# Kernel optimization log

Measured on AMD Instinct MI355X. Metric: run time of the kernel, lower is better.

The kernel has to match this reference:

```python
import jax, jax.numpy as jnp
import numpy as np

U, T, K, Q, H = 4096, 200, 64, 10000, 128
STD_THETA = 1.0


def setup_inputs() -> dict:
    key = jax.random.key(0)
    ks = jax.random.split(key, 12)
    q_id = jax.random.randint(ks[0], (U, T), 0, Q, dtype=jnp.int32)
    resp = jax.random.randint(ks[1], (U, T), 0, 2, dtype=jnp.int32)
    # one KC per question so the per-timestep masked_select size is constant (= U)
    kc_of_q = jax.random.randint(ks[2], (Q,), 0, K)
    kmap = jax.nn.one_hot(kc_of_q, K, dtype=jnp.float32) > 0.5  # (Q, K) bool, one-hot
    mask = jnp.ones((U, T), dtype=bool)
    diff_mu = jax.random.normal(ks[3], (Q,), dtype=jnp.float32)
    disc_mu = jax.random.normal(ks[4], (Q,), dtype=jnp.float32)
    xav = lambda k, fi, fo: jax.random.normal(k, (fi, fo), dtype=jnp.float32) * (2.0 / (fi + fo)) ** 0.5
    W1 = xav(ks[5], 3, H)
    W2 = xav(ks[6], H, H)
    W3 = xav(ks[7], H, 2)
    b1 = jnp.zeros((H,), jnp.float32)
    b2 = jnp.zeros((H,), jnp.float32)
    b3 = jnp.zeros((2,), jnp.float32)
    return dict(mask=mask, q_id=q_id, kmap=kmap, resp=resp,
                diff_mu=diff_mu, disc_mu=disc_mu,
                W1=W1, b1=b1, W2=W2, b2=b2, W3=W3, b3=b3)


def reference(mask, q_id, kmap, resp, diff_mu, disc_mu, W1, b1, W2, b2, W3, b3):
    gelu = lambda x: jax.nn.gelu(x, approximate=False)  # torch nn.GELU default = exact erf
    nu = q_id.shape[0]
    td = diff_mu[q_id]                      # (U, T) trial difficulty
    ts = disc_mu[q_id]                      # (U, T) trial discrimination
    x = jnp.stack([td, ts, resp.astype(jnp.float32)], axis=-1)  # (U, T, 3)
    h = gelu(gelu(x @ W1 + b1) @ W2 + b2)
    out = gelu(h @ W3 + b3)                 # (U, T, 2)
    mu = out[..., 0].T                      # (T, U)
    logvar = out[..., 1].T                  # (T, U)
    std = jnp.maximum(jnp.exp(0.5 * logvar), 1e-8)
    r = (STD_THETA / std) ** 2              # (T, U)

    # backward Kalman-style recursion: b_t = 1/(1 + r_t + (1 - b_{t+1})), c_t = b_t*(c_{t+1} + r_t*mu_t)
    def bwd_step(carry, rm):
        b_n, c_n = carry
        r_t, mu_t = rm
        b_t = 1.0 / (1.0 + r_t + (1.0 - b_n))
        c_t = b_t * (c_n + r_t * mu_t)
        return (b_t, c_t), (b_t, c_t)

    init = (jnp.ones((nu,), mu.dtype), jnp.zeros((nu,), mu.dtype))
    _, (b_seq, c_seq) = jax.lax.scan(bwd_step, init, (r, mu), reverse=True)  # (T, U) each

    # forward pass: gather active-KC ability, update, scatter back into per-user KC state
    active_kc = jnp.argmax(kmap[q_id], axis=-1).T  # (T, U) one active KC per trial
    uidx = jnp.arange(nu)

    def fwd_step(curr, bck):
        b_t, c_t, kc_t = bck
        prev = curr[uidx, kc_t]
        mu_t = b_t * prev + c_t
        curr = curr.at[uidx, kc_t].set(mu_t)
        return curr, mu_t

    curr0 = jnp.zeros((nu, kmap.shape[1]), mu.dtype)
    last_ability_kc, ability_T = jax.lax.scan(fwd_step, curr0, (b_seq, c_seq, active_kc))
    ability = ability_T.T                   # (U, T): masked mean over one-hot KC = active KC ability
    trial_logits = ts * (ability - td)      # (U, T)
    return trial_logits, last_ability_kc
```

## Files before the change

### kernel.cpp

```cpp
#include <hip/hip_runtime.h>
#include <math.h>

#define U_ 4096
#define T_ 200
#define K_ 64
#define Q_ 10000
#define H_ 128

__device__ __forceinline__ float gelu_f(float x) {
  return 0.5f * x * (1.0f + erff(x * 0.70710678118654752440f));
}

__device__ __forceinline__ float rlanef(float v, int l) {
  return __int_as_float(__builtin_amdgcn_readlane(__float_as_int(v), l));
}
__device__ __forceinline__ int rlanei(int v, int l) {
  return __builtin_amdgcn_readlane(v, l);
}

__global__ __launch_bounds__(256, 4) void mlp_table_kernel(
    const float* __restrict__ diff_mu, const float* __restrict__ disc_mu,
    const float* __restrict__ W1, const float* __restrict__ b1,
    const float* __restrict__ W2, const float* __restrict__ b2,
    const float* __restrict__ W3, const float* __restrict__ b3,
    const unsigned char* __restrict__ kmap,
    float4* __restrict__ tab4, int* __restrict__ kc_of_q) {
  __shared__ float W2s[64 * H_];
  __shared__ float h1buf[16][H_];

  const int tid = threadIdx.x;
  const int base = blockIdx.x * 16;

  for (int v = tid; v < 64 * H_; v += 256) W2s[v] = W2[v];

  if (blockIdx.x < 40) {
    int q = blockIdx.x * 256 + tid;
    if (q < Q_) {
      const unsigned char* km = kmap + (size_t)q * K_;
      int kc = 0;
#pragma unroll
      for (int k = 0; k < K_; ++k)
        if (km[k]) kc = k;
      kc_of_q[q] = kc;
    }
  }

  for (int v = tid; v < 16 * H_; v += 256) {
    int pl = v >> 7, j = v & 127;
    int pg = base + pl;
    int q = pg >> 1;
    float rf = (float)(pg & 1);
    float td = diff_mu[q], ts = disc_mu[q];
    float a = b1[j];
    a += td * W1[j];
    a += ts * W1[H_ + j];
    a += rf * W1[2 * H_ + j];
    h1buf[pl][j] = gelu_f(a);
  }
  __syncthreads();

  const int w = tid >> 6, lane = tid & 63;
  float a0[4] = {0.f, 0.f, 0.f, 0.f}, a1[4] = {0.f, 0.f, 0.f, 0.f};
  const float* h1w = &h1buf[w * 4][0];

#pragma clang loop unroll_count(8)
  for (int k = 0; k < 64; ++k) {
    float w0 = W2s[k * H_ + lane];
    float w1 = W2s[k * H_ + lane + 64];
#pragma unroll
    for (int p = 0; p < 4; ++p) {
      float hv = h1w[p * H_ + k];
      a0[p] = fmaf(w0, hv, a0[p]);
      a1[p] = fmaf(w1, hv, a1[p]);
    }
  }
  __syncthreads();
  for (int v = tid; v < 64 * H_; v += 256) W2s[v] = W2[64 * H_ + v];
  __syncthreads();
#pragma clang loop unroll_count(8)
  for (int k = 0; k < 64; ++k) {
    float w0 = W2s[k * H_ + lane];
    float w1 = W2s[k * H_ + lane + 64];
#pragma unroll
    for (int p = 0; p < 4; ++p) {
      float hv = h1w[p * H_ + 64 + k];
      a0[p] = fmaf(w0, hv, a0[p]);
      a1[p] = fmaf(w1, hv, a1[p]);
    }
  }

  float w30a = W3[lane * 2 + 0], w31a = W3[lane * 2 + 1];
  float w30b = W3[(lane + 64) * 2 + 0], w31b = W3[(lane + 64) * 2 + 1];
  float b2a = b2[lane], b2b = b2[lane + 64];
  float b30 = b3[0], b31 = b3[1];
#pragma unroll
  for (int p = 0; p < 4; ++p) {
    float h2a = gelu_f(a0[p] + b2a);
    float h2b = gelu_f(a1[p] + b2b);
    float s0 = h2a * w30a + h2b * w30b;
    float s1 = h2a * w31a + h2b * w31b;
#pragma unroll
    for (int off = 32; off > 0; off >>= 1) {
      s0 += __shfl_xor(s0, off, 64);
      s1 += __shfl_xor(s1, off, 64);
    }
    if (lane == 0) {
      float mu = gelu_f(s0 + b30);
      float lv = gelu_f(s1 + b31);
      float sd = fmaxf(expf(0.5f * lv), 1e-8f);
      int pg = base + w * 4 + p;
      int q = pg >> 1;
      tab4[pg] = make_float4(1.0f / (sd * sd), mu, disc_mu[q], diff_mu[q]);
    }
  }
}

__global__ __launch_bounds__(256) void scan_kernel(
    const int* __restrict__ q_id, const int* __restrict__ resp,
    const float4* __restrict__ tab4, const int* __restrict__ kc_of_q,
    float* __restrict__ out) {
  const int lane = threadIdx.x & 63;
  const int u = (blockIdx.x << 2) | (threadIdx.x >> 6);

  float tr[4], tmu[4], tts[4], ttd[4];
  int tkc[4];
#pragma unroll
  for (int i = 0; i < 4; ++i) {
    int t = i * 64 + lane;
    int tc = t < T_ ? t : T_ - 1;
    int q = q_id[u * T_ + tc];
    int rp = resp[u * T_ + tc];
    float4 f = tab4[q * 2 + rp];
    tr[i] = f.x;
    tmu[i] = f.y;
    tts[i] = f.z;
    ttd[i] = f.w;
    tkc[i] = kc_of_q[q];
  }

  float b = 1.0f, c = 0.0f;
#define BWD_STEP(i, s)                                   \
  {                                                      \
    float r_ = rlanef(tr[i], s);                         \
    float m_ = rlanef(tmu[i], s);                        \
    float x_ = 2.0f + r_ - b;                            \
    float ib = __builtin_amdgcn_rcpf(x_);                \
    ib = ib * (2.0f - x_ * ib);         \
    b = ib;                                              \
    c = b * fmaf(r_, m_, c);                             \
    tr[i] = (lane == (s)) ? b : tr[i];                   \
    tmu[i] = (lane == (s)) ? c : tmu[i];                 \
  }
#pragma unroll
  for (int s = 7; s >= 0; --s) BWD_STEP(3, s)
#pragma unroll
  for (int s = 63; s >= 0; --s) BWD_STEP(2, s)
#pragma unroll
  for (int s = 63; s >= 0; --s) BWD_STEP(1, s)
#pragma unroll
  for (int s = 63; s >= 0; --s) BWD_STEP(0, s)
#undef BWD_STEP

  float curr = 0.0f;
  float* logits = out;
  float* last = out + (size_t)U_ * T_;

#define FWD_STEP(i, s)                                    \
  {                                                       \
    float b_ = rlanef(tr[i], s);                          \
    float c_ = rlanef(tmu[i], s);                         \
    int kc_ = rlanei(tkc[i], s);                          \
    float ts_ = rlanef(tts[i], s);                        \
    float td_ = rlanef(ttd[i], s);                        \
    float prev = rlanef(curr, kc_);                       \
    float ab = fmaf(b_, prev, c_);                        \
    curr = (lane == kc_) ? ab : curr;                     \
    float lg = ts_ * (ab - td_);                          \
    lsave = (lane == (s)) ? lg : lsave;                   \
  }
  {
    float lsave = 0.0f;
#pragma unroll
    for (int s = 0; s < 64; ++s) FWD_STEP(0, s)
    logits[u * T_ + lane] = lsave;
  }
  {
    float lsave = 0.0f;
#pragma unroll
    for (int s = 0; s < 64; ++s) FWD_STEP(1, s)
    logits[u * T_ + 64 + lane] = lsave;
  }
  {
    float lsave = 0.0f;
#pragma unroll
    for (int s = 0; s < 64; ++s) FWD_STEP(2, s)
    logits[u * T_ + 128 + lane] = lsave;
  }
  {
    float lsave = 0.0f;
#pragma unroll
    for (int s = 0; s < 8; ++s) FWD_STEP(3, s)
    if (lane < 8) logits[u * T_ + 192 + lane] = lsave;
  }
#undef FWD_STEP

  last[u * K_ + lane] = curr;
}

extern "C" void kernel_launch(void* const* d_in, const int* in_sizes, int n_in,
                              void* d_out, int out_size, void* d_ws,
                              size_t ws_size, hipStream_t stream) {
  const int* q_id = (const int*)d_in[1];
  const unsigned char* kmap = (const unsigned char*)d_in[2];
  const int* resp = (const int*)d_in[3];
  const float* diff_mu = (const float*)d_in[4];
  const float* disc_mu = (const float*)d_in[5];
  const float* W1 = (const float*)d_in[6];
  const float* b1 = (const float*)d_in[7];
  const float* W2 = (const float*)d_in[8];
  const float* b2 = (const float*)d_in[9];
  const float* W3 = (const float*)d_in[10];
  const float* b3 = (const float*)d_in[11];
  float* out = (float*)d_out;
  char* ws = (char*)d_ws;

  auto align512 = [](size_t x) { return (x + 511) & ~(size_t)511; };
  size_t o = 0;
  float4* tab4 = (float4*)(ws + o);  o = align512(o + (size_t)2 * Q_ * 16);
  int* kc_of_q = (int*)(ws + o);     o = align512(o + (size_t)Q_ * 4);
  (void)ws_size; (void)in_sizes; (void)n_in; (void)out_size;

  mlp_table_kernel<<<1250, 256, 0, stream>>>(diff_mu, disc_mu, W1, b1, W2, b2,
                                             W3, b3, kmap, tab4, kc_of_q);
  scan_kernel<<<U_ / 4, 256, 0, stream>>>(q_id, resp, tab4, kc_of_q, out);
}
```

Before: 153.9 us.

## Batch 16 users per block and run per-lane scans through shared memory

Replaces the one-wavefront-per-user scan, which broadcast each timestep with lane reads, with a block that stages 16 users' (r, mu) pairs and KC indices in LDS. One lane per user then runs the backward and forward recursions serially, keeping the per-user KC state in padded shared memory. Logits and the final KC states are written afterwards by all threads. This removes the long chains of lane-read instructions, at the cost of far fewer active lanes and waves (one partly used wave per block), so each step becomes bound by LDS latency.

```diff
diff --git a/kernel.cpp b/kernel.cpp
--- a/kernel.cpp
+++ b/kernel.cpp
@@ -6,16 +6,10 @@
 #define K_ 64
 #define Q_ 10000
 #define H_ 128
+#define UPB 16
 
 __device__ __forceinline__ float gelu_f(float x) {
   return 0.5f * x * (1.0f + erff(x * 0.70710678118654752440f));
-}
-
-__device__ __forceinline__ float rlanef(float v, int l) {
-  return __int_as_float(__builtin_amdgcn_readlane(__float_as_int(v), l));
-}
-__device__ __forceinline__ int rlanei(int v, int l) {
-  return __builtin_amdgcn_readlane(v, l);
 }
 
 __global__ __launch_bounds__(256, 4) void mlp_table_kernel(
@@ -115,96 +109,86 @@
   }
 }
 
-__global__ __launch_bounds__(256) void scan_kernel(
+__global__ __launch_bounds__(256) void scan2_kernel(
     const int* __restrict__ q_id, const int* __restrict__ resp,
     const float4* __restrict__ tab4, const int* __restrict__ kc_of_q,
     float* __restrict__ out) {
-  const int lane = threadIdx.x & 63;
-  const int u = (blockIdx.x << 2) | (threadIdx.x >> 6);
-
-  float tr[4], tmu[4], tts[4], ttd[4];
-  int tkc[4];
-#pragma unroll
-  for (int i = 0; i < 4; ++i) {
-    int t = i * 64 + lane;
-    int tc = t < T_ ? t : T_ - 1;
-    int q = q_id[u * T_ + tc];
-    int rp = resp[u * T_ + tc];
-    float4 f = tab4[q * 2 + rp];
-    tr[i] = f.x;
-    tmu[i] = f.y;
-    tts[i] = f.z;
-    ttd[i] = f.w;
-    tkc[i] = kc_of_q[q];
-  }
-
-  float b = 1.0f, c = 0.0f;
-#define BWD_STEP(i, s)                                   \
-  {                                                      \
-    float r_ = rlanef(tr[i], s);                         \
-    float m_ = rlanef(tmu[i], s);                        \
-    float x_ = 2.0f + r_ - b;                            \
-    float ib = __builtin_amdgcn_rcpf(x_);                \
-    ib = ib * (2.0f - x_ * ib);         \
-    b = ib;                                              \
-    c = b * fmaf(r_, m_, c);                             \
-    tr[i] = (lane == (s)) ? b : tr[i];                   \
-    tmu[i] = (lane == (s)) ? c : tmu[i];                 \
-  }
-#pragma unroll
-  for (int s = 7; s >= 0; --s) BWD_STEP(3, s)
-#pragma unroll
-  for (int s = 63; s >= 0; --s) BWD_STEP(2, s)
-#pragma unroll
-  for (int s = 63; s >= 0; --s) BWD_STEP(1, s)
-#pragma unroll
-  for (int s = 63; s >= 0; --s) BWD_STEP(0, s)
-#undef BWD_STEP
-
-  float curr = 0.0f;
+  __shared__ float2 bcs[T_ * (UPB + 1)];
+  __shared__ unsigned char kcs[T_ * UPB];
+  __shared__ float states[UPB * (K_ + 1)];
+
+  const int tid = threadIdx.x;
+  const int lane = tid & 63;
+  const int wv = tid >> 6;
+  const int u0 = blockIdx.x * UPB;
+
+  for (int v = tid; v < UPB * (K_ + 1); v += 256) states[v] = 0.0f;
+
+  for (int uu = 0; uu < 4; ++uu) {
+    const int ul = wv * 4 + uu;
+    const int* qrow = q_id + (size_t)(u0 + ul) * T_;
+    const int* rrow = resp + (size_t)(u0 + ul) * T_;
+#pragma unroll
+    for (int tile = 0; tile < 4; ++tile) {
+      int t = tile * 64 + lane;
+      if (t < T_) {
+        int q = qrow[t];
+        int rp = rrow[t];
+        float4 f = tab4[q * 2 + rp];
+        bcs[t * (UPB + 1) + ul] = make_float2(f.x, f.y);
+        kcs[t * UPB + ul] = (unsigned char)kc_of_q[q];
+      }
+    }
+  }
+  __syncthreads();
+
+  if (wv == 0) {
+    const bool act = lane < UPB;
+    const int ll = act ? lane : 0;
+
+    float b = 1.0f, c = 0.0f;
+#pragma unroll 4
+    for (int t = T_ - 1; t >= 0; --t) {
+      float2 rm_ = bcs[t * (UPB + 1) + ll];
+      float x_ = 2.0f + rm_.x - b;
+      float ib = __builtin_amdgcn_rcpf(x_);
+      ib = ib * (2.0f - x_ * ib);
+      b = ib;
+      c = b * fmaf(rm_.x, rm_.y, c);
+      if (act) bcs[t * (UPB + 1) + lane] = make_float2(b, c);
+    }
+
+#pragma unroll 2
+    for (int t = 0; t < T_; ++t) {
+      float2 bc_ = bcs[t * (UPB + 1) + ll];
+      int kc = (int)kcs[t * UPB + ll];
+      float prev = states[ll * (K_ + 1) + kc];
+      float ab = fmaf(bc_.x, prev, bc_.y);
+      if (act) {
+        states[lane * (K_ + 1) + kc] = ab;
+        bcs[t * (UPB + 1) + lane].x = ab;
+      }
+    }
+  }
+  __syncthreads();
+
   float* logits = out;
   float* last = out + (size_t)U_ * T_;
 
-#define FWD_STEP(i, s)                                    \
-  {                                                       \
-    float b_ = rlanef(tr[i], s);                          \
-    float c_ = rlanef(tmu[i], s);                         \
-    int kc_ = rlanei(tkc[i], s);                          \
-    float ts_ = rlanef(tts[i], s);                        \
-    float td_ = rlanef(ttd[i], s);                        \
-    float prev = rlanef(curr, kc_);                       \
-    float ab = fmaf(b_, prev, c_);                        \
-    curr = (lane == kc_) ? ab : curr;                     \
-    float lg = ts_ * (ab - td_);                          \
-    lsave = (lane == (s)) ? lg : lsave;                   \
-  }
-  {
-    float lsave = 0.0f;
-#pragma unroll
-    for (int s = 0; s < 64; ++s) FWD_STEP(0, s)
-    logits[u * T_ + lane] = lsave;
-  }
-  {
-    float lsave = 0.0f;
-#pragma unroll
-    for (int s = 0; s < 64; ++s) FWD_STEP(1, s)
-    logits[u * T_ + 64 + lane] = lsave;
-  }
-  {
-    float lsave = 0.0f;
-#pragma unroll
-    for (int s = 0; s < 64; ++s) FWD_STEP(2, s)
-    logits[u * T_ + 128 + lane] = lsave;
-  }
-  {
-    float lsave = 0.0f;
-#pragma unroll
-    for (int s = 0; s < 8; ++s) FWD_STEP(3, s)
-    if (lane < 8) logits[u * T_ + 192 + lane] = lsave;
-  }
-#undef FWD_STEP
-
-  last[u * K_ + lane] = curr;
+  for (int ul = 0; ul < UPB; ++ul) {
+    if (tid < T_) {
+      const int gu = u0 + ul;
+      int q = q_id[(size_t)gu * T_ + tid];
+      int rp = resp[(size_t)gu * T_ + tid];
+      float4 f = tab4[q * 2 + rp];
+      float ab = bcs[tid * (UPB + 1) + ul].x;
+      logits[(size_t)gu * T_ + tid] = f.z * (ab - f.w);
+    }
+  }
+  for (int v = tid; v < UPB * K_; v += 256) {
+    int ul = v >> 6, kc = v & 63;
+    last[(size_t)(u0 + ul) * K_ + kc] = states[ul * (K_ + 1) + kc];
+  }
 }
 
 extern "C" void kernel_launch(void* const* d_in, const int* in_sizes, int n_in,
@@ -232,5 +216,5 @@
 
   mlp_table_kernel<<<1250, 256, 0, stream>>>(diff_mu, disc_mu, W1, b1, W2, b2,
                                              W3, b3, kmap, tab4, kc_of_q);
-  scan_kernel<<<U_ / 4, 256, 0, stream>>>(q_id, resp, tab4, kc_of_q, out);
-}
+  scan2_kernel<<<U_ / UPB, 256, 0, stream>>>(q_id, resp, tab4, kc_of_q, out);
+}
```

Result: faster. 141.1 us (-8.3%).
